# Kernel tuning notes

Measured on AMD Instinct MI355X. Metric: run time of the kernel, lower is better.

Reference implementation:

```python
import jax, jax.numpy as jnp
import numpy as np

N, E, G = 50000, 800000, 128
IN, HID, HEAD = 1280, 256, 4
DH = HID // HEAD
EPS = 1e-5
ATT_SCALE = 1.0 / np.sqrt(1280.0).astype(np.float32)  # hardcoded in source


def _seg_softmax(x, seg, n):
    # softmax over segments along axis 0; x: [K] or [K, H]
    m = jax.ops.segment_max(x, seg, num_segments=n)
    e = jnp.exp(x - m[seg])
    s = jax.ops.segment_sum(e, seg, num_segments=n)
    return e / s[seg]


def _bn(x, g, b):
    # eval-mode BatchNorm1d with init running stats (mean=0, var=1)
    return g * x * (1.0 / np.sqrt(1.0 + EPS)) + b


def _ln(x, g, b):
    mu = x.mean(-1, keepdims=True)
    var = ((x - mu) ** 2).mean(-1, keepdims=True)
    return g * (x - mu) / jnp.sqrt(var + EPS) + b


def setup_inputs() -> dict:
    key = jax.random.key(0)
    ks = jax.random.split(key, 40)
    rn = lambda i, shp, s=0.05: jax.random.normal(ks[i], shp, jnp.float32) * s
    inp = {
        "h": jax.random.normal(ks[0], (N, IN), jnp.float32),
        "gcn_w0": rn(1, (IN, HID)), "gcn_b0": rn(2, (HID,), 0.01),
        "gcn_w1": rn(3, (HID, HID)), "gcn_b1": rn(4, (HID,), 0.01),
        "bn_gcn0_g": 1.0 + rn(5, (HID,), 0.1), "bn_gcn0_b": rn(6, (HID,), 0.01),
        "bn_gcn1_g": 1.0 + rn(7, (HID,), 0.1), "bn_gcn1_b": rn(8, (HID,), 0.01),
        "gat_w0": rn(9, (IN, HID)), "gat_al0": rn(10, (HEAD, DH)), "gat_ar0": rn(11, (HEAD, DH)), "gat_bias0": rn(12, (HID,), 0.01),
        "gat_w1": rn(13, (HID, HID)), "gat_al1": rn(14, (HEAD, DH)), "gat_ar1": rn(15, (HEAD, DH)), "gat_bias1": rn(16, (HID,), 0.01),
        "bn_gat0_g": 1.0 + rn(17, (HID,), 0.1), "bn_gat0_b": rn(18, (HID,), 0.01),
        "bn_gat1_g": 1.0 + rn(19, (HID,), 0.1), "bn_gat1_b": rn(20, (HID,), 0.01),
        "gate_w": rn(21, (2 * HID, HID)), "gate_b": rn(22, (HID,), 0.01),
        "qw": rn(23, (HEAD, HID, HID)), "kw": rn(24, (HEAD, HID, HID)), "vw": rn(25, (HEAD, HID, HID)),
        "ct_w": rn(26, (HEAD * HID, HID)),
        "ff_w1": rn(27, (HID, 2 * HID)), "ff_b1": rn(28, (2 * HID,), 0.01),
        "ff_w2": rn(29, (2 * HID, HID)), "ff_b2": rn(30, (HID,), 0.01),
        "ln_g": 1.0 + rn(31, (HID,), 0.1), "ln_b": rn(32, (HID,), 0.01),
        "src": jax.random.randint(ks[33], (E,), 0, N, jnp.int32),
        "dst": jax.random.randint(ks[34], (E,), 0, N, jnp.int32),
        "gid": jnp.sort(jax.random.randint(ks[35], (N,), 0, G, jnp.int32)),
        "num_graphs": G,
    }
    return inp


def reference(h, gcn_w0, gcn_b0, gcn_w1, gcn_b1, bn_gcn0_g, bn_gcn0_b, bn_gcn1_g, bn_gcn1_b,
              gat_w0, gat_al0, gat_ar0, gat_bias0, gat_w1, gat_al1, gat_ar1, gat_bias1,
              bn_gat0_g, bn_gat0_b, bn_gat1_g, bn_gat1_b, gate_w, gate_b,
              qw, kw, vw, ct_w, ff_w1, ff_b1, ff_w2, ff_b2, ln_g, ln_b,
              src, dst, gid, num_graphs):
    n = h.shape[0]
    ones_e = jnp.ones(src.shape[0], h.dtype)
    # dgl.mean_nodes per graph
    cnt = jnp.clip(jax.ops.segment_sum(jnp.ones(n, h.dtype), gid, num_segments=num_graphs), 1.0)
    init_avg_h = jax.ops.segment_sum(h, gid, num_segments=num_graphs) / cnt[:, None]
    # GraphConv norm='both', degrees clamped to >=1
    deg_out = jnp.clip(jax.ops.segment_sum(ones_e, src, num_segments=n), 1.0)
    deg_in = jnp.clip(jax.ops.segment_sum(ones_e, dst, num_segments=n), 1.0)
    ns, nd = deg_out ** -0.5, deg_in ** -0.5

    def gcn(x, w, b):
        m = (x * ns[:, None]) @ w  # [N, HID]
        return jax.ops.segment_sum(m[src], dst, num_segments=n) * nd[:, None] + b

    hg = jax.nn.relu(_bn(gcn(h, gcn_w0, gcn_b0), bn_gcn0_g, bn_gcn0_b))
    hg = jax.nn.relu(_bn(gcn(hg, gcn_w1, gcn_b1), bn_gcn1_g, bn_gcn1_b)) + hg

    def gat(x, w, al, ar, b):
        f = (x @ w).reshape(n, HEAD, DH)
        el = (f * al).sum(-1)  # [N, HEAD]
        er = (f * ar).sum(-1)
        e = jax.nn.leaky_relu(el[src] + er[dst], 0.2)  # [E, HEAD]
        alpha = _seg_softmax(e, dst, n)  # edge softmax over incoming edges
        out = jax.ops.segment_sum(alpha[:, :, None] * f[src], dst, num_segments=n)
        return out.reshape(n, HID) + b

    ha = jax.nn.elu(_bn(gat(h, gat_w0, gat_al0, gat_ar0, gat_bias0), bn_gat0_g, bn_gat0_b))
    ha = jax.nn.elu(_bn(gat(ha, gat_w1, gat_al1, gat_ar1, gat_bias1), bn_gat1_g, bn_gat1_b)) + ha

    gate = jax.nn.sigmoid(jnp.concatenate([hg, ha], axis=1) @ gate_w + gate_b)
    x = gate * hg + (1.0 - gate) * ha  # residue_h

    # transformer_block: per-graph node softmax attention
    q = jnp.einsum('nd,hde->nhe', x, qw)
    k = jnp.einsum('nd,hde->nhe', x, kw)
    v = jnp.einsum('nd,hde->nhe', x, vw)
    att = (q * k).sum(-1) * ATT_SCALE  # [N, HEAD]
    alpha = _seg_softmax(att, gid, num_graphs)  # dgl.softmax_nodes per head
    mo = (v * alpha[:, :, None]).reshape(n, HEAD * HID) @ ct_w
    x1 = _ln(mo + x, ln_g, ln_b)
    x2 = _ln(jax.nn.relu(x1 @ ff_w1 + ff_b1) @ ff_w2 + ff_b2 + x1, ln_g, ln_b)

    readout = jax.ops.segment_sum(x2, gid, num_segments=num_graphs)
    return readout, init_avg_h
```

## Files before the change

### kernel.cpp

```cpp
#include <hip/hip_runtime.h>

#define NN 50000
#define NE 800000
#define NG 128
#define DIN 1280
#define HIDDEN 256
#define BNS 0.9999950000374997f
#define ATT_SCALE 0.027950849718747373f
#define LN_EPS 1e-5f

typedef __attribute__((ext_vector_type(8))) short short8;
typedef __attribute__((ext_vector_type(4))) float floatx4;

__device__ __forceinline__ float b2f(unsigned short u) {
  return __uint_as_float(((unsigned int)u) << 16);
}
__device__ __forceinline__ unsigned short f2b(float f) {
  unsigned int x = __float_as_uint(f);
  x += 0x7fffu + ((x >> 16) & 1u);
  return (unsigned short)(x >> 16);
}

__global__ void transpose_w_k(const float* __restrict__ src, unsigned short* __restrict__ dst,
                              int K, int Nc) {
  int idx = blockIdx.x * 256 + threadIdx.x;
  if (idx >= K * Nc) return;
  int n = idx / K, k = idx % K;
  dst[idx] = f2b(src[(size_t)k * Nc + n]);
}

__global__ void mw_k(const float* __restrict__ qw, const float* __restrict__ kw,
                     unsigned short* __restrict__ dst) {
  int col = blockIdx.x;
  int d = threadIdx.x;
  int hh = col >> 8, dp = col & 255;
  const float* qr = qw + ((size_t)hh * 256 + d) * 256;
  const float* kr = kw + ((size_t)hh * 256 + dp) * 256;
  float s = 0.f;
  for (int e = 0; e < 256; e += 4) {
    float4 a = *(const float4*)(qr + e);
    float4 b = *(const float4*)(kr + e);
    s += a.x * b.x + a.y * b.y + a.z * b.z + a.w * b.w;
  }
  dst[(size_t)col * 256 + d] = f2b(s);
}

__global__ void w2_k(const float* __restrict__ vw, const float* __restrict__ ctw,
                     unsigned short* __restrict__ dst) {
  int b = blockIdx.x;
  int c = threadIdx.x;
  int hh = b >> 8, d = b & 255;
  const float* vr = vw + ((size_t)hh * 256 + d) * 256;
  float s = 0.f;
  for (int e = 0; e < 256; ++e)
    s += vr[e] * ctw[(size_t)(hh * 256 + e) * 256 + c];
  dst[(size_t)c * 1024 + b] = f2b(s);
}

__global__ void cvt_avg_k(const float* __restrict__ h, const int* __restrict__ gid,
                          unsigned short* __restrict__ h_bf, float* __restrict__ out1) {
  int row0 = blockIdx.x * 50;
  int tid = threadIdx.x;
  float4 acc = {0.f, 0.f, 0.f, 0.f};
  int cur_g = gid[row0];
  int c4 = tid * 4;
  for (int r = 0; r < 50; ++r) {
    int row = row0 + r;
    int g = gid[row];
    if (g != cur_g) {
      atomicAdd(&out1[(size_t)cur_g * DIN + c4 + 0], acc.x);
      atomicAdd(&out1[(size_t)cur_g * DIN + c4 + 1], acc.y);
      atomicAdd(&out1[(size_t)cur_g * DIN + c4 + 2], acc.z);
      atomicAdd(&out1[(size_t)cur_g * DIN + c4 + 3], acc.w);
      acc = {0.f, 0.f, 0.f, 0.f};
      cur_g = g;
    }
    float4 v = *(const float4*)(h + (size_t)row * DIN + c4);
    acc.x += v.x; acc.y += v.y; acc.z += v.z; acc.w += v.w;
    ushort4 o;
    o.x = f2b(v.x); o.y = f2b(v.y); o.z = f2b(v.z); o.w = f2b(v.w);
    *(ushort4*)(h_bf + (size_t)row * DIN + c4) = o;
  }
  atomicAdd(&out1[(size_t)cur_g * DIN + c4 + 0], acc.x);
  atomicAdd(&out1[(size_t)cur_g * DIN + c4 + 1], acc.y);
  atomicAdd(&out1[(size_t)cur_g * DIN + c4 + 2], acc.z);
  atomicAdd(&out1[(size_t)cur_g * DIN + c4 + 3], acc.w);
}

__global__ void div_avg_k(const int* __restrict__ start, float* __restrict__ out1) {
  int idx = blockIdx.x * 256 + threadIdx.x;
  if (idx >= NG * DIN) return;
  int g = idx / DIN;
  float cnt = (float)(start[g + 1] - start[g]);
  if (cnt < 1.f) cnt = 1.f;
  out1[idx] /= cnt;
}

__global__ void graph_bounds_k(const int* __restrict__ gid, int* __restrict__ start, int n) {
  int i = blockIdx.x * 256 + threadIdx.x;
  if (i >= n) return;
  int g = gid[i];
  if (i == 0) {
    for (int gg = 0; gg <= g; ++gg) start[gg] = 0;
  } else {
    int gp = gid[i - 1];
    for (int gg = gp + 1; gg <= g; ++gg) start[gg] = i;
  }
  if (i == n - 1) {
    for (int gg = g + 1; gg <= NG; ++gg) start[gg] = n;
  }
}

__global__ void degrees_k(const int* __restrict__ src, const int* __restrict__ dst,
                          int* __restrict__ deg_out, int* __restrict__ deg_in, int e) {
  int i = blockIdx.x * 256 + threadIdx.x;
  if (i >= e) return;
  atomicAdd(&deg_out[src[i]], 1);
  atomicAdd(&deg_in[dst[i]], 1);
}

__global__ void invsqrt_k(const int* __restrict__ deg_out, const int* __restrict__ deg_in,
                          float* __restrict__ ns, float* __restrict__ nd, int n) {
  int i = blockIdx.x * 256 + threadIdx.x;
  if (i >= n) return;
  int a = deg_out[i]; if (a < 1) a = 1;
  int b = deg_in[i];  if (b < 1) b = 1;
  ns[i] = rsqrtf((float)a);
  nd[i] = rsqrtf((float)b);
}

__global__ void scan_local_k(const int* __restrict__ deg, int* __restrict__ row_ptr,
                             int* __restrict__ bsum) {
  __shared__ int buf[256];
  int b = blockIdx.x, t = threadIdx.x;
  int i = b * 256 + t;
  int v = (i < NN) ? deg[i] : 0;
  buf[t] = v;
  __syncthreads();
  for (int off = 1; off < 256; off <<= 1) {
    int tv = (t >= off) ? buf[t - off] : 0;
    __syncthreads();
    buf[t] += tv;
    __syncthreads();
  }
  if (i < NN) row_ptr[i] = buf[t] - v;
  if (t == 255) bsum[b] = buf[255];
}

__global__ void scan_bsum_k(int* __restrict__ bsum, int* __restrict__ boff, int nb,
                            int* __restrict__ row_ptr) {
  __shared__ int buf[256];
  int t = threadIdx.x;
  int v = (t < nb) ? bsum[t] : 0;
  buf[t] = v;
  __syncthreads();
  for (int off = 1; off < 256; off <<= 1) {
    int tv = (t >= off) ? buf[t - off] : 0;
    __syncthreads();
    buf[t] += tv;
    __syncthreads();
  }
  if (t < nb) boff[t] = buf[t] - v;
  if (t == 0) row_ptr[NN] = NE;
}

__global__ void scan_add_k(int* __restrict__ row_ptr, const int* __restrict__ boff) {
  int i = blockIdx.x * 256 + threadIdx.x;
  if (i >= NN) return;
  row_ptr[i] += boff[blockIdx.x];
}

__global__ void fill_csr_k(const int* __restrict__ src, const int* __restrict__ dst,
                           const int* __restrict__ row_ptr, int* __restrict__ fill,
                           int* __restrict__ csr_src, int e) {
  int i = blockIdx.x * 256 + threadIdx.x;
  if (i >= e) return;
  int d = dst[i];
  int pos = row_ptr[d] + atomicAdd(&fill[d], 1);
  csr_src[pos] = src[i];
}

template <int MODE>
__global__ __launch_bounds__(256, 2) void gemm_bf16(const unsigned short* __restrict__ A,
                                                    const unsigned short* __restrict__ Bt,
                                                    void* __restrict__ Cout,
                                                    const float* __restrict__ bias,
                                                    int M, int K, int Nc,
                                                    const unsigned short* __restrict__ xtile,
                                                    float* __restrict__ attp,
                                                    const float* __restrict__ ascale,
                                                    const float* __restrict__ al,
                                                    const float* __restrict__ ar,
                                                    float* __restrict__ elr,
                                                    int ecol0) {
  __shared__ unsigned short sbuf[32768];
  const int tid = threadIdx.x;
  const int n0 = blockIdx.x * 128;
  const int m0 = blockIdx.y * 128;
  const int w = tid >> 6;
  const int lane = tid & 63;
  const int wr = (w >> 1) * 64;
  const int wc = (w & 1) * 64;
  const int quad = lane >> 4;
  const int l15 = lane & 15;
  const int js = tid & 7;
  const int mbase = tid >> 3;
  const int wbase = w * 64;

  bool do_elr = (MODE == 8);
  const unsigned short* Ap = A;
  const unsigned short* Bp = Bt;
  unsigned short* Cp = (unsigned short*)Cout;
  if (MODE == 8 && gridDim.z == 2) {
    if (blockIdx.z == 0) {
      do_elr = false;
    } else {
      Ap += 12800000;
      Bp += 65536;
      Cp += 12800000;
    }
  }

  floatx4 acc[4][4];
#pragma unroll
  for (int i = 0; i < 4; ++i)
#pragma unroll
    for (int j = 0; j < 4; ++j) acc[i][j] = (floatx4)0.0f;

  if constexpr (MODE == 6) {
    unsigned short* lA = sbuf;
    unsigned short* lB = sbuf + 8192;
    for (int k0 = 0; k0 < K; k0 += 64) {
      __syncthreads();
#pragma unroll
      for (int it = 0; it < 4; ++it) {
        int m = it * 32 + mbase;
        int gm = m0 + m;
        if (gm >= M) gm = M - 1;
        uint4 va = *(const uint4*)(Ap + (size_t)gm * 256 + (k0 & 255) + js * 8);
        float s = ascale[(size_t)gm * 4 + (k0 >> 8)];
        unsigned short* pp = (unsigned short*)&va;
#pragma unroll
        for (int c = 0; c < 8; ++c) pp[c] = f2b(b2f(pp[c]) * s);
        *(uint4*)(lA + (size_t)(m * 8 + (js ^ (m & 7))) * 8) = va;
      }
#pragma unroll
      for (int it = 0; it < 4; ++it) {
        int c = it * 256 + wbase + lane;
        int m = c >> 3, g = c & 7;
        int gn = n0 + m;
        const unsigned short* gp = Bp + (size_t)gn * K + k0 + (g ^ (m & 7)) * 8;
        __builtin_amdgcn_global_load_lds(
            (const __attribute__((address_space(1))) unsigned int*)gp,
            (__attribute__((address_space(3))) unsigned int*)(lB + (size_t)(it * 256 + wbase) * 8),
            16, 0, 0);
      }
      __syncthreads();
#pragma unroll
      for (int ks = 0; ks < 2; ++ks) {
        int kb = ks * 4 + quad;
        short8 af[4], bfr[4];
#pragma unroll
        for (int ri = 0; ri < 4; ++ri) {
          int r = wr + ri * 16 + l15;
          af[ri] = *(const short8*)(lA + (size_t)(r * 8 + (kb ^ (r & 7))) * 8);
        }
#pragma unroll
        for (int ci = 0; ci < 4; ++ci) {
          int c = wc + ci * 16 + l15;
          bfr[ci] = *(const short8*)(lB + (size_t)(c * 8 + (kb ^ (c & 7))) * 8);
        }
#pragma unroll
        for (int ri = 0; ri < 4; ++ri)
#pragma unroll
          for (int ci = 0; ci < 4; ++ci)
            acc[ri][ci] = __builtin_amdgcn_mfma_f32_16x16x32_bf16(af[ri], bfr[ci], acc[ri][ci], 0, 0, 0);
      }
    }
    __syncthreads();
  } else {
    const int nt = K >> 6;
    auto stage = [&](int b, int k0) {
      unsigned short* lA = sbuf + b * 16384;
      unsigned short* lB = lA + 8192;
#pragma unroll
      for (int it = 0; it < 4; ++it) {
        int c = it * 256 + wbase + lane;
        int m = c >> 3, g = c & 7;
        int gm = m0 + m;
        if (gm >= M) gm = M - 1;
        const unsigned short* gp = Ap + (size_t)gm * K + k0 + (g ^ (m & 7)) * 8;
        __builtin_amdgcn_global_load_lds(
            (const __attribute__((address_space(1))) unsigned int*)gp,
            (__attribute__((address_space(3))) unsigned int*)(lA + (size_t)(it * 256 + wbase) * 8),
            16, 0, 0);
      }
#pragma unroll
      for (int it = 0; it < 4; ++it) {
        int c = it * 256 + wbase + lane;
        int m = c >> 3, g = c & 7;
        int gn = n0 + m;
        const unsigned short* gp = Bp + (size_t)gn * K + k0 + (g ^ (m & 7)) * 8;
        __builtin_amdgcn_global_load_lds(
            (const __attribute__((address_space(1))) unsigned int*)gp,
            (__attribute__((address_space(3))) unsigned int*)(lB + (size_t)(it * 256 + wbase) * 8),
            16, 0, 0);
      }
    };
    stage(0, 0);
    __syncthreads();
    for (int t = 0; t < nt; ++t) {
      int cur = t & 1;
      if (t + 1 < nt) stage(cur ^ 1, (t + 1) * 64);
      unsigned short* lA = sbuf + cur * 16384;
      unsigned short* lB = lA + 8192;
#pragma unroll
      for (int ks = 0; ks < 2; ++ks) {
        int kb = ks * 4 + quad;
        short8 af[4], bfr[4];
#pragma unroll
        for (int ri = 0; ri < 4; ++ri) {
          int r = wr + ri * 16 + l15;
          af[ri] = *(const short8*)(lA + (size_t)(r * 8 + (kb ^ (r & 7))) * 8);
        }
#pragma unroll
        for (int ci = 0; ci < 4; ++ci) {
          int c = wc + ci * 16 + l15;
          bfr[ci] = *(const short8*)(lB + (size_t)(c * 8 + (kb ^ (c & 7))) * 8);
        }
#pragma unroll
        for (int ri = 0; ri < 4; ++ri)
#pragma unroll
          for (int ci = 0; ci < 4; ++ci)
            acc[ri][ci] = __builtin_amdgcn_mfma_f32_16x16x32_bf16(af[ri], bfr[ci], acc[ri][ci], 0, 0, 0);
      }
      __syncthreads();
    }
  }

  if (MODE == 4) {
    int cb = n0 & 255;
#pragma unroll
    for (int it2 = 0; it2 < 8; ++it2) {
      int linear = it2 * 256 + tid;
      int rr = linear >> 4;
      int c8 = (linear & 15) * 8;
      int gr = m0 + rr;
      if (gr >= M) gr = M - 1;
      *(uint4*)(sbuf + rr * 128 + c8) = *(const uint4*)(xtile + (size_t)gr * 256 + cb + c8);
    }
    __syncthreads();
    int head = n0 >> 8;
#pragma unroll
    for (int ri = 0; ri < 4; ++ri) {
      int lrow = wr + ri * 16 + quad * 4;
#pragma unroll
      for (int r = 0; r < 4; ++r) {
        float p = 0.f;
#pragma unroll
        for (int ci = 0; ci < 4; ++ci)
          p += acc[ri][ci][r] * b2f(sbuf[(lrow + r) * 128 + wc + ci * 16 + l15]);
        p += __shfl_xor(p, 1);
        p += __shfl_xor(p, 2);
        p += __shfl_xor(p, 4);
        p += __shfl_xor(p, 8);
        if (l15 == 0) {
          int grow = m0 + lrow + r;
          if (grow < M) atomicAdd(&attp[(size_t)grow * 4 + head], p * ATT_SCALE);
        }
      }
    }
    return;
  }

  if (MODE == 7) {
#pragma unroll
    for (int ri = 0; ri < 4; ++ri) {
      int row = m0 + wr + ri * 16 + quad * 4;
#pragma unroll
      for (int ci = 0; ci < 4; ++ci) {
        int col = n0 + wc + ci * 16 + l15;
        float bv = bias[col];
#pragma unroll
        for (int r = 0; r < 4; ++r) {
          if (row + r < M) {
            float g = 1.f / (1.f + expf(-(acc[ri][ci][r] + bv)));
            float hg = b2f(xtile[(size_t)(row + r) * 512 + col]);
            float ha = b2f(xtile[(size_t)(row + r) * 512 + 256 + col]);
            Cp[(size_t)(row + r) * Nc + col] = f2b(g * hg + (1.f - g) * ha);
          }
        }
      }
    }
    return;
  }

  if (MODE == 8 && do_elr && n0 >= ecol0) {
    int head = (n0 - ecol0 + wc) >> 6;
#pragma unroll
    for (int ri = 0; ri < 4; ++ri) {
      int lrow = wr + ri * 16 + quad * 4;
#pragma unroll
      for (int r = 0; r < 4; ++r) {
        float pl = 0.f, pr = 0.f;
#pragma unroll
        for (int ci = 0; ci < 4; ++ci) {
          float fv = acc[ri][ci][r];
          pl += fv * al[head * 64 + ci * 16 + l15];
          pr += fv * ar[head * 64 + ci * 16 + l15];
        }
        pl += __shfl_xor(pl, 1); pl += __shfl_xor(pl, 2);
        pl += __shfl_xor(pl, 4); pl += __shfl_xor(pl, 8);
        pr += __shfl_xor(pr, 1); pr += __shfl_xor(pr, 2);
        pr += __shfl_xor(pr, 4); pr += __shfl_xor(pr, 8);
        if (l15 == 0) {
          int grow = m0 + lrow + r;
          if (grow < M) {
            elr[(size_t)grow * 8 + head] = pl;
            elr[(size_t)grow * 8 + 4 + head] = pr;
          }
        }
      }
    }
  }

#pragma unroll
  for (int ri = 0; ri < 4; ++ri) {
    int row = m0 + wr + ri * 16 + quad * 4;
#pragma unroll
    for (int ci = 0; ci < 4; ++ci) {
      int col = n0 + wc + ci * 16 + l15;
      float bv = (MODE == 2) ? bias[col] : 0.f;
#pragma unroll
      for (int r = 0; r < 4; ++r) {
        if (row + r < M) {
          float v = acc[ri][ci][r];
          if (MODE == 2) { v += bv; v = fmaxf(v, 0.f); }
          if (MODE == 1)
            ((float*)Cout)[(size_t)(row + r) * Nc + col] = v;
          else
            Cp[(size_t)(row + r) * Nc + col] = f2b(v);
        }
      }
    }
  }
}

__global__ void gcn_agg_k(const unsigned short* __restrict__ m, int ldm,
                          const int* __restrict__ row_ptr, const int* __restrict__ csr_src,
                          const float* __restrict__ ns, const float* __restrict__ nd,
                          const float* __restrict__ bias,
                          const float* __restrict__ bng, const float* __restrict__ bnb,
                          const unsigned short* __restrict__ resid, int ldr,
                          unsigned short* __restrict__ out, int ldo) {
  int node = blockIdx.x * 4 + (threadIdx.x >> 6);
  if (node >= NN) return;
  int lane = threadIdx.x & 63;
  int s = row_ptr[node], e = row_ptr[node + 1];
  float a0 = 0, a1 = 0, a2 = 0, a3 = 0;
  for (int i = s; i < e; ++i) {
    int u = csr_src[i];
    float w = ns[u];
    ushort4 v = *(const ushort4*)(m + (size_t)u * ldm + lane * 4);
    a0 += w * b2f(v.x); a1 += w * b2f(v.y); a2 += w * b2f(v.z); a3 += w * b2f(v.w);
  }
  float ndv = nd[node];
  int col = lane * 4;
  float vals[4] = {a0, a1, a2, a3};
  ushort4 o;
#pragma unroll
  for (int c = 0; c < 4; ++c) {
    float v = vals[c] * ndv + bias[col + c];
    v = bng[col + c] * v * BNS + bnb[col + c];
    v = fmaxf(v, 0.f);
    if (resid) v += b2f(resid[(size_t)node * ldr + col + c]);
    ((unsigned short*)&o)[c] = f2b(v);
  }
  *(ushort4*)(out + (size_t)node * ldo + col) = o;
}

__global__ void gat_agg_k(const unsigned short* __restrict__ f, int ldf,
                          const int* __restrict__ row_ptr, const int* __restrict__ csr_src,
                          const float* __restrict__ elr,
                          const float* __restrict__ bias,
                          const float* __restrict__ bng, const float* __restrict__ bnb,
                          const unsigned short* __restrict__ resid, int ldr,
                          unsigned short* __restrict__ out, int ldo) {
  int node = blockIdx.x * 4 + (threadIdx.x >> 6);
  if (node >= NN) return;
  int lane = threadIdx.x & 63;
  int s = row_ptr[node], e = row_ptr[node + 1];
  float4 er = *(const float4*)(elr + (size_t)node * 8 + 4);
  float m0 = -1e30f, m1 = -1e30f, m2 = -1e30f, m3 = -1e30f;
  for (int i = s + lane; i < e; i += 64) {
    int u = csr_src[i];
    float4 el = *(const float4*)(elr + (size_t)u * 8);
    float t;
    t = el.x + er.x; t = t > 0.f ? t : 0.2f * t; m0 = fmaxf(m0, t);
    t = el.y + er.y; t = t > 0.f ? t : 0.2f * t; m1 = fmaxf(m1, t);
    t = el.z + er.z; t = t > 0.f ? t : 0.2f * t; m2 = fmaxf(m2, t);
    t = el.w + er.w; t = t > 0.f ? t : 0.2f * t; m3 = fmaxf(m3, t);
  }
#pragma unroll
  for (int off = 1; off < 64; off <<= 1) {
    m0 = fmaxf(m0, __shfl_xor(m0, off));
    m1 = fmaxf(m1, __shfl_xor(m1, off));
    m2 = fmaxf(m2, __shfl_xor(m2, off));
    m3 = fmaxf(m3, __shfl_xor(m3, off));
  }
  float s0 = 0, s1 = 0, s2 = 0, s3 = 0;
  for (int i = s + lane; i < e; i += 64) {
    int u = csr_src[i];
    float4 el = *(const float4*)(elr + (size_t)u * 8);
    float t;
    t = el.x + er.x; t = t > 0.f ? t : 0.2f * t; s0 += expf(t - m0);
    t = el.y + er.y; t = t > 0.f ? t : 0.2f * t; s1 += expf(t - m1);
    t = el.z + er.z; t = t > 0.f ? t : 0.2f * t; s2 += expf(t - m2);
    t = el.w + er.w; t = t > 0.f ? t : 0.2f * t; s3 += expf(t - m3);
  }
#pragma unroll
  for (int off = 1; off < 64; off <<= 1) {
    s0 += __shfl_xor(s0, off);
    s1 += __shfl_xor(s1, off);
    s2 += __shfl_xor(s2, off);
    s3 += __shfl_xor(s3, off);
  }
  int head = lane >> 4;
  float erh = head == 0 ? er.x : head == 1 ? er.y : head == 2 ? er.z : er.w;
  float mh = head == 0 ? m0 : head == 1 ? m1 : head == 2 ? m2 : m3;
  float sh = head == 0 ? s0 : head == 1 ? s1 : head == 2 ? s2 : s3;
  float inv_sh = (sh > 0.f) ? 1.f / sh : 0.f;
  float a0 = 0, a1 = 0, a2 = 0, a3 = 0;
  for (int i = s; i < e; ++i) {
    int u = csr_src[i];
    float t = elr[(size_t)u * 8 + head] + erh;
    t = t > 0.f ? t : 0.2f * t;
    float wgt = expf(t - mh) * inv_sh;
    ushort4 v = *(const ushort4*)(f + (size_t)u * ldf + lane * 4);
    a0 += wgt * b2f(v.x); a1 += wgt * b2f(v.y); a2 += wgt * b2f(v.z); a3 += wgt * b2f(v.w);
  }
  int col = lane * 4;
  float vals[4] = {a0, a1, a2, a3};
  ushort4 o;
#pragma unroll
  for (int c = 0; c < 4; ++c) {
    float v = vals[c] + bias[col + c];
    v = bng[col + c] * v * BNS + bnb[col + c];
    v = (v > 0.f) ? v : (expf(v) - 1.f);
    if (resid) v += b2f(resid[(size_t)node * ldr + col + c]);
    ((unsigned short*)&o)[c] = f2b(v);
  }
  *(ushort4*)(out + (size_t)node * ldo + col) = o;
}

__global__ void gsoftmax_k(const float* __restrict__ att, const int* __restrict__ start,
                           float* __restrict__ alpha) {
  int g = blockIdx.x;
  int s = start[g], e = start[g + 1];
  int tid = threadIdx.x;
  __shared__ float red[256];
  __shared__ float mh[4], sh[4];
  float lm[4] = {-1e30f, -1e30f, -1e30f, -1e30f};
  for (int i = s + tid; i < e; i += 256) {
    float4 a = *(const float4*)(att + (size_t)i * 4);
    lm[0] = fmaxf(lm[0], a.x); lm[1] = fmaxf(lm[1], a.y);
    lm[2] = fmaxf(lm[2], a.z); lm[3] = fmaxf(lm[3], a.w);
  }
#pragma unroll
  for (int h = 0; h < 4; ++h) {
    red[tid] = lm[h]; __syncthreads();
    for (int off = 128; off > 0; off >>= 1) {
      if (tid < off) red[tid] = fmaxf(red[tid], red[tid + off]);
      __syncthreads();
    }
    if (tid == 0) mh[h] = red[0];
    __syncthreads();
  }
  float ls[4] = {0, 0, 0, 0};
  for (int i = s + tid; i < e; i += 256) {
    float4 a = *(const float4*)(att + (size_t)i * 4);
    ls[0] += expf(a.x - mh[0]); ls[1] += expf(a.y - mh[1]);
    ls[2] += expf(a.z - mh[2]); ls[3] += expf(a.w - mh[3]);
  }
#pragma unroll
  for (int h = 0; h < 4; ++h) {
    red[tid] = ls[h]; __syncthreads();
    for (int off = 128; off > 0; off >>= 1) {
      if (tid < off) red[tid] += red[tid + off];
      __syncthreads();
    }
    if (tid == 0) sh[h] = red[0];
    __syncthreads();
  }
  for (int i = s + tid; i < e; i += 256) {
    float4 a = *(const float4*)(att + (size_t)i * 4);
    float4 o;
    o.x = expf(a.x - mh[0]) / sh[0];
    o.y = expf(a.y - mh[1]) / sh[1];
    o.z = expf(a.z - mh[2]) / sh[2];
    o.w = expf(a.w - mh[3]) / sh[3];
    *(float4*)(alpha + (size_t)i * 4) = o;
  }
}

__global__ void ln1_k(const unsigned short* __restrict__ mo, const unsigned short* __restrict__ x,
                      const float* __restrict__ g, const float* __restrict__ b,
                      unsigned short* __restrict__ x1) {
  int node = blockIdx.x * 4 + (threadIdx.x >> 6);
  if (node >= NN) return;
  int lane = threadIdx.x & 63;
  int c = lane * 4;
  ushort4 a = *(const ushort4*)(mo + (size_t)node * HIDDEN + c);
  ushort4 xx = *(const ushort4*)(x + (size_t)node * HIDDEN + c);
  float v0 = b2f(a.x) + b2f(xx.x), v1 = b2f(a.y) + b2f(xx.y);
  float v2 = b2f(a.z) + b2f(xx.z), v3 = b2f(a.w) + b2f(xx.w);
  float sm = v0 + v1 + v2 + v3;
#pragma unroll
  for (int off = 1; off < 64; off <<= 1) sm += __shfl_xor(sm, off);
  float mu = sm * (1.f / 256.f);
  float d0 = v0 - mu, d1 = v1 - mu, d2 = v2 - mu, d3 = v3 - mu;
  float sq = d0 * d0 + d1 * d1 + d2 * d2 + d3 * d3;
#pragma unroll
  for (int off = 1; off < 64; off <<= 1) sq += __shfl_xor(sq, off);
  float inv = rsqrtf(sq * (1.f / 256.f) + LN_EPS);
  ushort4 ob;
  ob.x = f2b(g[c + 0] * d0 * inv + b[c + 0]);
  ob.y = f2b(g[c + 1] * d1 * inv + b[c + 1]);
  ob.z = f2b(g[c + 2] * d2 * inv + b[c + 2]);
  ob.w = f2b(g[c + 3] * d3 * inv + b[c + 3]);
  *(ushort4*)(x1 + (size_t)node * HIDDEN + c) = ob;
}

__global__ void ln2_k(const unsigned short* __restrict__ ff2o, const float* __restrict__ ffb2,
                      const unsigned short* __restrict__ x1,
                      const float* __restrict__ g, const float* __restrict__ b,
                      unsigned short* __restrict__ x2) {
  int node = blockIdx.x * 4 + (threadIdx.x >> 6);
  if (node >= NN) return;
  int lane = threadIdx.x & 63;
  int c = lane * 4;
  ushort4 a = *(const ushort4*)(ff2o + (size_t)node * HIDDEN + c);
  ushort4 xx = *(const ushort4*)(x1 + (size_t)node * HIDDEN + c);
  float v0 = b2f(a.x) + ffb2[c + 0] + b2f(xx.x), v1 = b2f(a.y) + ffb2[c + 1] + b2f(xx.y);
  float v2 = b2f(a.z) + ffb2[c + 2] + b2f(xx.z), v3 = b2f(a.w) + ffb2[c + 3] + b2f(xx.w);
  float sm = v0 + v1 + v2 + v3;
#pragma unroll
  for (int off = 1; off < 64; off <<= 1) sm += __shfl_xor(sm, off);
  float mu = sm * (1.f / 256.f);
  float d0 = v0 - mu, d1 = v1 - mu, d2 = v2 - mu, d3 = v3 - mu;
  float sq = d0 * d0 + d1 * d1 + d2 * d2 + d3 * d3;
#pragma unroll
  for (int off = 1; off < 64; off <<= 1) sq += __shfl_xor(sq, off);
  float inv = rsqrtf(sq * (1.f / 256.f) + LN_EPS);
  ushort4 ob;
  ob.x = f2b(g[c + 0] * d0 * inv + b[c + 0]);
  ob.y = f2b(g[c + 1] * d1 * inv + b[c + 1]);
  ob.z = f2b(g[c + 2] * d2 * inv + b[c + 2]);
  ob.w = f2b(g[c + 3] * d3 * inv + b[c + 3]);
  *(ushort4*)(x2 + (size_t)node * HIDDEN + c) = ob;
}

__global__ void readout_k(const unsigned short* __restrict__ x2, const int* __restrict__ start,
                          float* __restrict__ out0) {
  int g = blockIdx.x;
  int c = threadIdx.x;
  float acc = 0.f;
  for (int i = start[g]; i < start[g + 1]; ++i) acc += b2f(x2[(size_t)i * HIDDEN + c]);
  out0[(size_t)g * HIDDEN + c] = acc;
}

static const size_t OFF_BUFA   = 0;
static const size_t OFF_C01    = 128000000;
static const size_t OFF_HG0    = 179200000;
static const size_t OFF_HA0    = 204800000;
static const size_t OFF_M1     = 230400000;
static const size_t OFF_F1     = 256000000;
static const size_t OFF_XCAT   = 281600000;
static const size_t OFF_GLOGIT = 332800000;
static const size_t OFF_XB     = 358400000;
static const size_t OFF_MO     = 384000000;
static const size_t OFF_X1     = 409600000;
static const size_t OFF_ATT    = 435200000;
static const size_t OFF_ALPHA  = OFF_ATT + 800000;
static const size_t OFF_ELR0   = OFF_ALPHA + 800000;
static const size_t OFF_ELR1   = OFF_ELR0 + 1600000;
static const size_t OFF_START  = OFF_ELR1 + 1600000;
static const size_t OFF_DEGO   = OFF_START + 1024;
static const size_t OFF_DEGI   = OFF_DEGO + 200704;
static const size_t OFF_NS     = OFF_DEGI + 200704;
static const size_t OFF_ND     = OFF_NS + 200704;
static const size_t OFF_ROWP   = OFF_ND + 200704;
static const size_t OFF_FILL   = OFF_ROWP + 200704;
static const size_t OFF_BSUM   = OFF_FILL + 200704;
static const size_t OFF_BOFF   = OFF_BSUM + 1024;
static const size_t OFF_CSRS   = OFF_BOFF + 1024;
static const size_t OFF_W01T   = OFF_CSRS + 3200000;
static const size_t OFF_W1T    = OFF_W01T + 1310720;
static const size_t OFF_W1GT   = OFF_W1T + 131072;
static const size_t OFF_GATEWT = OFF_W1GT + 131072;
static const size_t OFF_WMVT   = OFF_GATEWT + 262144;
static const size_t OFF_CTWT   = OFF_WMVT + 1048576;
static const size_t OFF_FFW1T  = OFF_CTWT + 524288;
static const size_t OFF_FFW2T  = OFF_FFW1T + 262144;
static const size_t WS_NEED    = OFF_FFW2T + 262144;

extern "C" void kernel_launch(void* const* d_in, const int* in_sizes, int n_in,
                              void* d_out, int out_size, void* d_ws, size_t ws_size,
                              hipStream_t stream) {
  if (ws_size < WS_NEED) return;

  const float* h       = (const float*)d_in[0];
  const float* gcn_w0  = (const float*)d_in[1];
  const float* gcn_b0  = (const float*)d_in[2];
  const float* gcn_w1  = (const float*)d_in[3];
  const float* gcn_b1  = (const float*)d_in[4];
  const float* bn_gcn0_g = (const float*)d_in[5];
  const float* bn_gcn0_b = (const float*)d_in[6];
  const float* bn_gcn1_g = (const float*)d_in[7];
  const float* bn_gcn1_b = (const float*)d_in[8];
  const float* gat_w0  = (const float*)d_in[9];
  const float* gat_al0 = (const float*)d_in[10];
  const float* gat_ar0 = (const float*)d_in[11];
  const float* gat_bias0 = (const float*)d_in[12];
  const float* gat_w1  = (const float*)d_in[13];
  const float* gat_al1 = (const float*)d_in[14];
  const float* gat_ar1 = (const float*)d_in[15];
  const float* gat_bias1 = (const float*)d_in[16];
  const float* bn_gat0_g = (const float*)d_in[17];
  const float* bn_gat0_b = (const float*)d_in[18];
  const float* bn_gat1_g = (const float*)d_in[19];
  const float* bn_gat1_b = (const float*)d_in[20];
  const float* gate_w  = (const float*)d_in[21];
  const float* gate_b  = (const float*)d_in[22];
  const float* qw      = (const float*)d_in[23];
  const float* kw      = (const float*)d_in[24];
  const float* vw      = (const float*)d_in[25];
  const float* ct_w    = (const float*)d_in[26];
  const float* ff_w1   = (const float*)d_in[27];
  const float* ff_b1   = (const float*)d_in[28];
  const float* ff_w2   = (const float*)d_in[29];
  const float* ff_b2   = (const float*)d_in[30];
  const float* ln_g    = (const float*)d_in[31];
  const float* ln_b    = (const float*)d_in[32];
  const int* srcv = (const int*)d_in[33];
  const int* dstv = (const int*)d_in[34];
  const int* gid  = (const int*)d_in[35];

  char* ws = (char*)d_ws;
  unsigned short* h_bf = (unsigned short*)(ws + OFF_BUFA);
  unsigned short* ff1o = (unsigned short*)(ws + OFF_BUFA);
  unsigned short* ff2o = (unsigned short*)(ws + OFF_BUFA + 51200000);
  unsigned short* x2   = (unsigned short*)(ws + OFF_BUFA + 76800000);
  unsigned short* c01  = (unsigned short*)(ws + OFF_C01);
  unsigned short* hg0  = (unsigned short*)(ws + OFF_HG0);
  unsigned short* ha0  = (unsigned short*)(ws + OFF_HA0);
  unsigned short* m1   = (unsigned short*)(ws + OFF_M1);
  unsigned short* f1   = (unsigned short*)(ws + OFF_F1);
  unsigned short* xcat = (unsigned short*)(ws + OFF_XCAT);
  unsigned short* xb   = (unsigned short*)(ws + OFF_XB);
  unsigned short* mo   = (unsigned short*)(ws + OFF_MO);
  unsigned short* x1   = (unsigned short*)(ws + OFF_X1);
  float* att           = (float*)(ws + OFF_ATT);
  float* alpha         = (float*)(ws + OFF_ALPHA);
  float* elr0          = (float*)(ws + OFF_ELR0);
  float* elr1          = (float*)(ws + OFF_ELR1);
  int* start   = (int*)(ws + OFF_START);
  int* deg_out = (int*)(ws + OFF_DEGO);
  int* deg_in  = (int*)(ws + OFF_DEGI);
  float* ns    = (float*)(ws + OFF_NS);
  float* nd    = (float*)(ws + OFF_ND);
  int* row_ptr = (int*)(ws + OFF_ROWP);
  int* fill    = (int*)(ws + OFF_FILL);
  int* bsum    = (int*)(ws + OFF_BSUM);
  int* boff    = (int*)(ws + OFF_BOFF);
  int* csr_src = (int*)(ws + OFF_CSRS);
  unsigned short* w01t   = (unsigned short*)(ws + OFF_W01T);
  unsigned short* w1t    = (unsigned short*)(ws + OFF_W1T);
  unsigned short* w1gt   = (unsigned short*)(ws + OFF_W1GT);
  unsigned short* gatewt = (unsigned short*)(ws + OFF_GATEWT);
  unsigned short* wmvt   = (unsigned short*)(ws + OFF_WMVT);
  unsigned short* w2t    = (unsigned short*)(ws + OFF_CTWT);
  unsigned short* ffw1t  = (unsigned short*)(ws + OFF_FFW1T);
  unsigned short* ffw2t  = (unsigned short*)(ws + OFF_FFW2T);

  float* out0 = (float*)d_out;
  float* out1 = out0 + NG * HIDDEN;

  hipMemsetAsync(deg_out, 0, NN * 4, stream);
  hipMemsetAsync(deg_in, 0, NN * 4, stream);
  hipMemsetAsync(fill, 0, NN * 4, stream);
  hipMemsetAsync(out1, 0, NG * DIN * 4, stream);
  hipMemsetAsync(att, 0, NN * 4 * 4, stream);

  transpose_w_k<<<(1280 * 256 + 255) / 256, 256, 0, stream>>>(gcn_w0, w01t, 1280, 256);
  transpose_w_k<<<(1280 * 256 + 255) / 256, 256, 0, stream>>>(gat_w0, w01t + 256 * 1280, 1280, 256);
  transpose_w_k<<<(256 * 256 + 255) / 256, 256, 0, stream>>>(gcn_w1, w1t, 256, 256);
  transpose_w_k<<<(256 * 256 + 255) / 256, 256, 0, stream>>>(gat_w1, w1gt, 256, 256);
  transpose_w_k<<<(512 * 256 + 255) / 256, 256, 0, stream>>>(gate_w, gatewt, 512, 256);
  mw_k<<<1024, 256, 0, stream>>>(qw, kw, wmvt);
  w2_k<<<1024, 256, 0, stream>>>(vw, ct_w, w2t);
  transpose_w_k<<<(256 * 512 + 255) / 256, 256, 0, stream>>>(ff_w1, ffw1t, 256, 512);
  transpose_w_k<<<(512 * 256 + 255) / 256, 256, 0, stream>>>(ff_w2, ffw2t, 512, 256);

  graph_bounds_k<<<(NN + 255) / 256, 256, 0, stream>>>(gid, start, NN);
  degrees_k<<<(NE + 255) / 256, 256, 0, stream>>>(srcv, dstv, deg_out, deg_in, NE);
  invsqrt_k<<<(NN + 255) / 256, 256, 0, stream>>>(deg_out, deg_in, ns, nd, NN);
  const int NB_SCAN = (NN + 255) / 256;
  scan_local_k<<<NB_SCAN, 256, 0, stream>>>(deg_in, row_ptr, bsum);
  scan_bsum_k<<<1, 256, 0, stream>>>(bsum, boff, NB_SCAN, row_ptr);
  scan_add_k<<<NB_SCAN, 256, 0, stream>>>(row_ptr, boff);
  fill_csr_k<<<(NE + 255) / 256, 256, 0, stream>>>(srcv, dstv, row_ptr, fill, csr_src, NE);

  cvt_avg_k<<<NN / 50, 320, 0, stream>>>(h, gid, h_bf, out1);
  div_avg_k<<<(NG * DIN + 255) / 256, 256, 0, stream>>>(start, out1);

  const int MB = (NN + 127) / 128;
  gemm_bf16<8><<<dim3(4, MB), 256, 0, stream>>>(h_bf, w01t, c01, nullptr, NN, 1280, 512,
                                                nullptr, nullptr, nullptr,
                                                gat_al0, gat_ar0, elr0, 256);
  gcn_agg_k<<<NN / 4, 256, 0, stream>>>(c01, 512, row_ptr, csr_src, ns, nd,
                                        gcn_b0, bn_gcn0_g, bn_gcn0_b, nullptr, 0, hg0, 256);
  gat_agg_k<<<NN / 4, 256, 0, stream>>>(c01 + 256, 512, row_ptr, csr_src, elr0,
                                        gat_bias0, bn_gat0_g, bn_gat0_b, nullptr, 0, ha0, 256);
  gemm_bf16<8><<<dim3(2, MB, 2), 256, 0, stream>>>(hg0, w1t, m1, nullptr, NN, 256, 256,
                                                   nullptr, nullptr, nullptr,
                                                   gat_al1, gat_ar1, elr1, 0);
  gcn_agg_k<<<NN / 4, 256, 0, stream>>>(m1, 256, row_ptr, csr_src, ns, nd,
                                        gcn_b1, bn_gcn1_g, bn_gcn1_b, hg0, 256, xcat, 512);
  gat_agg_k<<<NN / 4, 256, 0, stream>>>(f1, 256, row_ptr, csr_src, elr1,
                                        gat_bias1, bn_gat1_g, bn_gat1_b, ha0, 256, xcat + 256, 512);
  gemm_bf16<7><<<dim3(2, MB), 256, 0, stream>>>(xcat, gatewt, xb, gate_b, NN, 512, 256,
                                                xcat, nullptr, nullptr,
                                                nullptr, nullptr, nullptr, 0);
  gemm_bf16<4><<<dim3(8, MB), 256, 0, stream>>>(xb, wmvt, nullptr, nullptr, NN, 256, 1024,
                                                xb, att, nullptr,
                                                nullptr, nullptr, nullptr, 0);
  gsoftmax_k<<<NG, 256, 0, stream>>>(att, start, alpha);
  gemm_bf16<6><<<dim3(2, MB), 256, 0, stream>>>(xb, w2t, mo, nullptr, NN, 1024, 256,
                                                nullptr, nullptr, alpha,
                                                nullptr, nullptr, nullptr, 0);
  ln1_k<<<NN / 4, 256, 0, stream>>>(mo, xb, ln_g, ln_b, x1);
  gemm_bf16<2><<<dim3(4, MB), 256, 0, stream>>>(x1, ffw1t, ff1o, ff_b1, NN, 256, 512,
                                                nullptr, nullptr, nullptr,
                                                nullptr, nullptr, nullptr, 0);
  gemm_bf16<0><<<dim3(2, MB), 256, 0, stream>>>(ff1o, ffw2t, ff2o, nullptr, NN, 512, 256,
                                                nullptr, nullptr, nullptr,
                                                nullptr, nullptr, nullptr, 0);
  ln2_k<<<NN / 4, 256, 0, stream>>>(ff2o, ff_b2, x1, ln_g, ln_b, x2);
  readout_k<<<NG, 256, 0, stream>>>(x2, start, out0);
}
```

Baseline: 1.678 ms.

## Merge prep kernels, fuse degree/bounds/invsqrt, batch edge index loads in aggregation

Nine weight-prep launches become one kernel that picks its job from the block index. Graph bounds and degree counting are merged into one kernel, and the inverse-sqrt normalisation moves into the local scan. The three zero-fills become a single memset over a now-contiguous workspace region. In the GCN and GAT aggregation kernels, each 16-lane group loads up to 16 edge indices and weights at once and shares them with shuffles, instead of every lane loading them serially per edge. Together this removes launch overhead and redundant per-edge index and weight loads, at the cost of some shuffle work and imbalance across the merged blocks.

Result: faster. 1.576 ms (-6.1%).

```diff
diff --git a/kernel.cpp b/kernel.cpp
--- a/kernel.cpp
+++ b/kernel.cpp
@@ -21,40 +21,58 @@
   return (unsigned short)(x >> 16);
 }
 
-__global__ void transpose_w_k(const float* __restrict__ src, unsigned short* __restrict__ dst,
-                              int K, int Nc) {
-  int idx = blockIdx.x * 256 + threadIdx.x;
+__device__ __forceinline__ void tr_dev(const float* __restrict__ src,
+                                       unsigned short* __restrict__ dst,
+                                       int K, int Nc, int bi) {
+  int idx = bi * 256 + threadIdx.x;
   if (idx >= K * Nc) return;
   int n = idx / K, k = idx % K;
   dst[idx] = f2b(src[(size_t)k * Nc + n]);
 }
 
-__global__ void mw_k(const float* __restrict__ qw, const float* __restrict__ kw,
-                     unsigned short* __restrict__ dst) {
-  int col = blockIdx.x;
-  int d = threadIdx.x;
-  int hh = col >> 8, dp = col & 255;
-  const float* qr = qw + ((size_t)hh * 256 + d) * 256;
-  const float* kr = kw + ((size_t)hh * 256 + dp) * 256;
-  float s = 0.f;
-  for (int e = 0; e < 256; e += 4) {
-    float4 a = *(const float4*)(qr + e);
-    float4 b = *(const float4*)(kr + e);
-    s += a.x * b.x + a.y * b.y + a.z * b.z + a.w * b.w;
-  }
-  dst[(size_t)col * 256 + d] = f2b(s);
-}
-
-__global__ void w2_k(const float* __restrict__ vw, const float* __restrict__ ctw,
-                     unsigned short* __restrict__ dst) {
+__global__ void prep_all_k(const float* __restrict__ gcn_w0, const float* __restrict__ gat_w0,
+                           const float* __restrict__ gcn_w1, const float* __restrict__ gat_w1,
+                           const float* __restrict__ gate_w, const float* __restrict__ ff_w1,
+                           const float* __restrict__ ff_w2, const float* __restrict__ qw,
+                           const float* __restrict__ kw, const float* __restrict__ vw,
+                           const float* __restrict__ ctw,
+                           unsigned short* __restrict__ w01t, unsigned short* __restrict__ w1t,
+                           unsigned short* __restrict__ w1gt, unsigned short* __restrict__ gatewt,
+                           unsigned short* __restrict__ ffw1t, unsigned short* __restrict__ ffw2t,
+                           unsigned short* __restrict__ wmvt, unsigned short* __restrict__ w2t) {
   int b = blockIdx.x;
-  int c = threadIdx.x;
-  int hh = b >> 8, d = b & 255;
-  const float* vr = vw + ((size_t)hh * 256 + d) * 256;
-  float s = 0.f;
-  for (int e = 0; e < 256; ++e)
-    s += vr[e] * ctw[(size_t)(hh * 256 + e) * 256 + c];
-  dst[(size_t)c * 1024 + b] = f2b(s);
+  if (b < 1280) { tr_dev(gcn_w0, w01t, 1280, 256, b); return; }
+  if (b < 2560) { tr_dev(gat_w0, w01t + 256 * 1280, 1280, 256, b - 1280); return; }
+  if (b < 2816) { tr_dev(gcn_w1, w1t, 256, 256, b - 2560); return; }
+  if (b < 3072) { tr_dev(gat_w1, w1gt, 256, 256, b - 2816); return; }
+  if (b < 3584) { tr_dev(gate_w, gatewt, 512, 256, b - 3072); return; }
+  if (b < 4096) { tr_dev(ff_w1, ffw1t, 256, 512, b - 3584); return; }
+  if (b < 4608) { tr_dev(ff_w2, ffw2t, 512, 256, b - 4096); return; }
+  if (b < 5632) {
+    int col = b - 4608;
+    int d = threadIdx.x;
+    int hh = col >> 8, dp = col & 255;
+    const float* qr = qw + ((size_t)hh * 256 + d) * 256;
+    const float* kr = kw + ((size_t)hh * 256 + dp) * 256;
+    float s = 0.f;
+    for (int e = 0; e < 256; e += 4) {
+      float4 a = *(const float4*)(qr + e);
+      float4 bb = *(const float4*)(kr + e);
+      s += a.x * bb.x + a.y * bb.y + a.z * bb.z + a.w * bb.w;
+    }
+    wmvt[(size_t)col * 256 + d] = f2b(s);
+    return;
+  }
+  {
+    int bb = b - 5632;
+    int c = threadIdx.x;
+    int hh = bb >> 8, d = bb & 255;
+    const float* vr = vw + ((size_t)hh * 256 + d) * 256;
+    float s = 0.f;
+    for (int e = 0; e < 256; ++e)
+      s += vr[e] * ctw[(size_t)(hh * 256 + e) * 256 + c];
+    w2t[(size_t)c * 1024 + bb] = f2b(s);
+  }
 }
 
 __global__ void cvt_avg_k(const float* __restrict__ h, const int* __restrict__ gid,
@@ -96,45 +114,35 @@
   out1[idx] /= cnt;
 }
 
-__global__ void graph_bounds_k(const int* __restrict__ gid, int* __restrict__ start, int n) {
+__global__ void bounds_deg_k(const int* __restrict__ gid, int* __restrict__ start,
+                             const int* __restrict__ src, const int* __restrict__ dst,
+                             int* __restrict__ deg_out, int* __restrict__ deg_in) {
   int i = blockIdx.x * 256 + threadIdx.x;
-  if (i >= n) return;
-  int g = gid[i];
-  if (i == 0) {
-    for (int gg = 0; gg <= g; ++gg) start[gg] = 0;
-  } else {
-    int gp = gid[i - 1];
-    for (int gg = gp + 1; gg <= g; ++gg) start[gg] = i;
-  }
-  if (i == n - 1) {
-    for (int gg = g + 1; gg <= NG; ++gg) start[gg] = n;
-  }
-}
-
-__global__ void degrees_k(const int* __restrict__ src, const int* __restrict__ dst,
-                          int* __restrict__ deg_out, int* __restrict__ deg_in, int e) {
-  int i = blockIdx.x * 256 + threadIdx.x;
-  if (i >= e) return;
-  atomicAdd(&deg_out[src[i]], 1);
-  atomicAdd(&deg_in[dst[i]], 1);
-}
-
-__global__ void invsqrt_k(const int* __restrict__ deg_out, const int* __restrict__ deg_in,
-                          float* __restrict__ ns, float* __restrict__ nd, int n) {
-  int i = blockIdx.x * 256 + threadIdx.x;
-  if (i >= n) return;
-  int a = deg_out[i]; if (a < 1) a = 1;
-  int b = deg_in[i];  if (b < 1) b = 1;
-  ns[i] = rsqrtf((float)a);
-  nd[i] = rsqrtf((float)b);
-}
-
-__global__ void scan_local_k(const int* __restrict__ deg, int* __restrict__ row_ptr,
-                             int* __restrict__ bsum) {
+  if (i < NN) {
+    int g = gid[i];
+    if (i == 0) {
+      for (int gg = 0; gg <= g; ++gg) start[gg] = 0;
+    } else {
+      int gp = gid[i - 1];
+      for (int gg = gp + 1; gg <= g; ++gg) start[gg] = i;
+    }
+    if (i == NN - 1) {
+      for (int gg = g + 1; gg <= NG; ++gg) start[gg] = NN;
+    }
+  }
+  if (i < NE) {
+    atomicAdd(&deg_out[src[i]], 1);
+    atomicAdd(&deg_in[dst[i]], 1);
+  }
+}
+
+__global__ void scan_local_k(const int* __restrict__ deg_in, const int* __restrict__ deg_out,
+                             int* __restrict__ row_ptr, int* __restrict__ bsum,
+                             float* __restrict__ ns, float* __restrict__ nd) {
   __shared__ int buf[256];
   int b = blockIdx.x, t = threadIdx.x;
   int i = b * 256 + t;
-  int v = (i < NN) ? deg[i] : 0;
+  int v = (i < NN) ? deg_in[i] : 0;
   buf[t] = v;
   __syncthreads();
   for (int off = 1; off < 256; off <<= 1) {
@@ -143,7 +151,13 @@
     buf[t] += tv;
     __syncthreads();
   }
-  if (i < NN) row_ptr[i] = buf[t] - v;
+  if (i < NN) {
+    row_ptr[i] = buf[t] - v;
+    int a = deg_out[i]; if (a < 1) a = 1;
+    int bb = v;         if (bb < 1) bb = 1;
+    ns[i] = rsqrtf((float)a);
+    nd[i] = rsqrtf((float)bb);
+  }
   if (t == 255) bsum[b] = buf[255];
 }
 
@@ -457,12 +471,22 @@
   if (node >= NN) return;
   int lane = threadIdx.x & 63;
   int s = row_ptr[node], e = row_ptr[node + 1];
+  int eidx = lane & 15;
   float a0 = 0, a1 = 0, a2 = 0, a3 = 0;
-  for (int i = s; i < e; ++i) {
-    int u = csr_src[i];
-    float w = ns[u];
-    ushort4 v = *(const ushort4*)(m + (size_t)u * ldm + lane * 4);
-    a0 += w * b2f(v.x); a1 += w * b2f(v.y); a2 += w * b2f(v.z); a3 += w * b2f(v.w);
+  for (int i0 = s; i0 < e; i0 += 16) {
+    int n16 = e - i0; if (n16 > 16) n16 = 16;
+    int u_mine = 0; float w_mine = 0.f;
+    if (eidx < n16) {
+      u_mine = csr_src[i0 + eidx];
+      w_mine = ns[u_mine];
+    }
+    for (int e2 = 0; e2 < n16; ++e2) {
+      int sl = (lane & 48) | e2;
+      int u = __shfl(u_mine, sl);
+      float w = __shfl(w_mine, sl);
+      ushort4 v = *(const ushort4*)(m + (size_t)u * ldm + lane * 4);
+      a0 += w * b2f(v.x); a1 += w * b2f(v.y); a2 += w * b2f(v.z); a3 += w * b2f(v.w);
+    }
   }
   float ndv = nd[node];
   int col = lane * 4;
@@ -530,14 +554,25 @@
   float mh = head == 0 ? m0 : head == 1 ? m1 : head == 2 ? m2 : m3;
   float sh = head == 0 ? s0 : head == 1 ? s1 : head == 2 ? s2 : s3;
   float inv_sh = (sh > 0.f) ? 1.f / sh : 0.f;
+  int eidx = lane & 15;
   float a0 = 0, a1 = 0, a2 = 0, a3 = 0;
-  for (int i = s; i < e; ++i) {
-    int u = csr_src[i];
-    float t = elr[(size_t)u * 8 + head] + erh;
-    t = t > 0.f ? t : 0.2f * t;
-    float wgt = expf(t - mh) * inv_sh;
-    ushort4 v = *(const ushort4*)(f + (size_t)u * ldf + lane * 4);
-    a0 += wgt * b2f(v.x); a1 += wgt * b2f(v.y); a2 += wgt * b2f(v.z); a3 += wgt * b2f(v.w);
+  for (int i0 = s; i0 < e; i0 += 16) {
+    int n16 = e - i0; if (n16 > 16) n16 = 16;
+    int u_mine = 0; float w_mine = 0.f;
+    if (eidx < n16) {
+      u_mine = csr_src[i0 + eidx];
+      float el = elr[(size_t)u_mine * 8 + head];
+      float t = el + erh;
+      t = t > 0.f ? t : 0.2f * t;
+      w_mine = expf(t - mh) * inv_sh;
+    }
+    for (int e2 = 0; e2 < n16; ++e2) {
+      int sl = (lane & 48) | e2;
+      int u = __shfl(u_mine, sl);
+      float wgt = __shfl(w_mine, sl);
+      ushort4 v = *(const ushort4*)(f + (size_t)u * ldf + lane * 4);
+      a0 += wgt * b2f(v.x); a1 += wgt * b2f(v.y); a2 += wgt * b2f(v.z); a3 += wgt * b2f(v.w);
+    }
   }
   int col = lane * 4;
   float vals[4] = {a0, a1, a2, a3};
@@ -676,7 +711,6 @@
 static const size_t OFF_M1     = 230400000;
 static const size_t OFF_F1     = 256000000;
 static const size_t OFF_XCAT   = 281600000;
-static const size_t OFF_GLOGIT = 332800000;
 static const size_t OFF_XB     = 358400000;
 static const size_t OFF_MO     = 384000000;
 static const size_t OFF_X1     = 409600000;
@@ -687,11 +721,11 @@
 static const size_t OFF_START  = OFF_ELR1 + 1600000;
 static const size_t OFF_DEGO   = OFF_START + 1024;
 static const size_t OFF_DEGI   = OFF_DEGO + 200704;
-static const size_t OFF_NS     = OFF_DEGI + 200704;
+static const size_t OFF_FILL   = OFF_DEGI + 200704;
+static const size_t OFF_NS     = OFF_FILL + 200704;
 static const size_t OFF_ND     = OFF_NS + 200704;
 static const size_t OFF_ROWP   = OFF_ND + 200704;
-static const size_t OFF_FILL   = OFF_ROWP + 200704;
-static const size_t OFF_BSUM   = OFF_FILL + 200704;
+static const size_t OFF_BSUM   = OFF_ROWP + 200704;
 static const size_t OFF_BOFF   = OFF_BSUM + 1024;
 static const size_t OFF_CSRS   = OFF_BOFF + 1024;
 static const size_t OFF_W01T   = OFF_CSRS + 3200000;
@@ -767,10 +801,10 @@
   int* start   = (int*)(ws + OFF_START);
   int* deg_out = (int*)(ws + OFF_DEGO);
   int* deg_in  = (int*)(ws + OFF_DEGI);
+  int* fill    = (int*)(ws + OFF_FILL);
   float* ns    = (float*)(ws + OFF_NS);
   float* nd    = (float*)(ws + OFF_ND);
   int* row_ptr = (int*)(ws + OFF_ROWP);
-  int* fill    = (int*)(ws + OFF_FILL);
   int* bsum    = (int*)(ws + OFF_BSUM);
   int* boff    = (int*)(ws + OFF_BOFF);
   int* csr_src = (int*)(ws + OFF_CSRS);
@@ -786,27 +820,17 @@
   float* out0 = (float*)d_out;
   float* out1 = out0 + NG * HIDDEN;
 
-  hipMemsetAsync(deg_out, 0, NN * 4, stream);
-  hipMemsetAsync(deg_in, 0, NN * 4, stream);
-  hipMemsetAsync(fill, 0, NN * 4, stream);
+  hipMemsetAsync(deg_out, 0, 3 * 200704, stream);
   hipMemsetAsync(out1, 0, NG * DIN * 4, stream);
   hipMemsetAsync(att, 0, NN * 4 * 4, stream);
 
-  transpose_w_k<<<(1280 * 256 + 255) / 256, 256, 0, stream>>>(gcn_w0, w01t, 1280, 256);
-  transpose_w_k<<<(1280 * 256 + 255) / 256, 256, 0, stream>>>(gat_w0, w01t + 256 * 1280, 1280, 256);
-  transpose_w_k<<<(256 * 256 + 255) / 256, 256, 0, stream>>>(gcn_w1, w1t, 256, 256);
-  transpose_w_k<<<(256 * 256 + 255) / 256, 256, 0, stream>>>(gat_w1, w1gt, 256, 256);
-  transpose_w_k<<<(512 * 256 + 255) / 256, 256, 0, stream>>>(gate_w, gatewt, 512, 256);
-  mw_k<<<1024, 256, 0, stream>>>(qw, kw, wmvt);
-  w2_k<<<1024, 256, 0, stream>>>(vw, ct_w, w2t);
-  transpose_w_k<<<(256 * 512 + 255) / 256, 256, 0, stream>>>(ff_w1, ffw1t, 256, 512);
-  transpose_w_k<<<(512 * 256 + 255) / 256, 256, 0, stream>>>(ff_w2, ffw2t, 512, 256);
-
-  graph_bounds_k<<<(NN + 255) / 256, 256, 0, stream>>>(gid, start, NN);
-  degrees_k<<<(NE + 255) / 256, 256, 0, stream>>>(srcv, dstv, deg_out, deg_in, NE);
-  invsqrt_k<<<(NN + 255) / 256, 256, 0, stream>>>(deg_out, deg_in, ns, nd, NN);
+  prep_all_k<<<6656, 256, 0, stream>>>(gcn_w0, gat_w0, gcn_w1, gat_w1, gate_w, ff_w1, ff_w2,
+                                       qw, kw, vw, ct_w,
+                                       w01t, w1t, w1gt, gatewt, ffw1t, ffw2t, wmvt, w2t);
+
+  bounds_deg_k<<<(NE + 255) / 256, 256, 0, stream>>>(gid, start, srcv, dstv, deg_out, deg_in);
   const int NB_SCAN = (NN + 255) / 256;
-  scan_local_k<<<NB_SCAN, 256, 0, stream>>>(deg_in, row_ptr, bsum);
+  scan_local_k<<<NB_SCAN, 256, 0, stream>>>(deg_in, deg_out, row_ptr, bsum, ns, nd);
   scan_bsum_k<<<1, 256, 0, stream>>>(bsum, boff, NB_SCAN, row_ptr);
   scan_add_k<<<NB_SCAN, 256, 0, stream>>>(row_ptr, boff);
   fill_csr_k<<<(NE + 255) / 256, 256, 0, stream>>>(srcv, dstv, row_ptr, fill, csr_src, NE);
```
